# Kernel optimization log

Measured on AMD Instinct MI355X. Metric: run time of the kernel, lower is better.

Reference implementation:

```python
import jax, jax.numpy as jnp
import numpy as np

HIDDEN = 2048
NUM_HEADS = 16
HEAD_DIM = HIDDEN // NUM_HEADS


def setup_inputs() -> dict:
    key = jax.random.key(0)
    k1, k2, k3 = jax.random.split(key, 3)
    hidden_states = jax.random.normal(k1, (4, 2048, HIDDEN), dtype=jnp.float32)
    # torch Linear weight is (out, in); y = x @ W.T. Store transposed (in, out).
    w_qkv = jax.random.normal(k2, (HIDDEN, 3 * HIDDEN), dtype=jnp.float32) * (HIDDEN ** -0.5)
    w_o = jax.random.normal(k3, (HIDDEN, HIDDEN), dtype=jnp.float32) * (HIDDEN ** -0.5)
    return {"hidden_states": hidden_states, "w_qkv": w_qkv, "w_o": w_o}


def reference(hidden_states, w_qkv, w_o):
    B, S, _ = hidden_states.shape
    qkv = hidden_states @ w_qkv  # (B, S, 3*HIDDEN)
    # Faithful to torch .view: row-major reshape straight to (B, H, S, 3*head_dim)
    qkv = qkv.reshape(B, NUM_HEADS, S, 3 * HEAD_DIM)
    q, k, v = jnp.split(qkv, 3, axis=-1)  # each (B, H, S, head_dim)
    scores = jnp.einsum('bhsd,bhtd->bhst', q, k) / (HEAD_DIM ** 0.5)
    probs = jax.nn.softmax(scores, axis=-1)
    attn = jnp.einsum('bhst,bhtd->bhsd', probs, v)  # (B, H, S, head_dim)
    # Faithful to torch .reshape(B, S, hidden) without transpose
    attn = attn.reshape(B, S, HIDDEN)
    return attn @ w_o
```

## Files before the change

kernel.cpp:

```cpp
#include <hip/hip_runtime.h>
#include <stdint.h>

#define DEVINL __device__ __forceinline__

typedef __attribute__((ext_vector_type(8))) __bf16 bf16x8;
typedef __attribute__((ext_vector_type(4))) float f32x4;
typedef __attribute__((ext_vector_type(16))) float f32x16;

static constexpr int HID  = 2048;
static constexpr int NQ   = 6144;
static constexpr int SEQ  = 2048;
static constexpr int NB   = 4;
static constexpr int MTOT = NB * SEQ;

DEVINL unsigned short f2bf(float f) {
  union { float f; uint32_t u; } x; x.f = f;
  uint32_t r = x.u + 0x7fffu + ((x.u >> 16) & 1u);
  return (unsigned short)(r >> 16);
}

typedef const __attribute__((address_space(1))) void gvoid_t;
typedef __attribute__((address_space(3))) void svoid_t;

DEVINL void gload_lds16(const void* g, void* s) {
  __builtin_amdgcn_global_load_lds((gvoid_t*)(uintptr_t)g,
                                   (svoid_t*)(uint32_t)(uintptr_t)s,
                                   16, 0, 0);
}


__global__ void k_cvt(const float* __restrict__ in, unsigned short* __restrict__ out, int n4) {
  int i = blockIdx.x * blockDim.x + threadIdx.x;
  if (i >= n4) return;
  float4 v = ((const float4*)in)[i];
  ushort4 o;
  o.x = f2bf(v.x); o.y = f2bf(v.y); o.z = f2bf(v.z); o.w = f2bf(v.w);
  ((ushort4*)out)[i] = o;
}

__global__ void k_transpose_cvt(const float* __restrict__ in, unsigned short* __restrict__ out,
                                int R, int C) {
  __shared__ float tile[32][33];
  int c0 = blockIdx.x * 32, r0 = blockIdx.y * 32;
  int tx = threadIdx.x & 31, ty = threadIdx.x >> 5;
  #pragma unroll
  for (int i = 0; i < 32; i += 8)
    tile[ty + i][tx] = in[(size_t)(r0 + ty + i) * C + (c0 + tx)];
  __syncthreads();
  #pragma unroll
  for (int i = 0; i < 32; i += 8)
    out[(size_t)(c0 + ty + i) * R + (r0 + tx)] = f2bf(tile[tx][ty + i]);
}


template <int OUT_BF16>
__global__ __launch_bounds__(256, 2) void k_gemm(const unsigned short* __restrict__ A,
                                                 const unsigned short* __restrict__ BT,
                                                 void* __restrict__ Cout,
                                                 int M, int N, int K) {
  __shared__ unsigned short As[128 * 64];
  __shared__ unsigned short Bs[128 * 64];
  const int tid = threadIdx.x;
  const int w = tid >> 6, l = tid & 63;
  const int lane16 = l & 15, lgrp = l >> 4;
  const int bn = blockIdx.x, bm = blockIdx.y;
  const int wr = w >> 1, wc = w & 1;
  const int srow = l >> 3;
  const int sk = (l & 7) * 8;

  f32x4 acc[4][4] = {};

  for (int k0 = 0; k0 < K; k0 += 64) {
    #pragma unroll
    for (int i = 0; i < 4; ++i) {
      const int chunk = i * 4 + w;
      const int row = chunk * 8 + srow;
      gload_lds16(A  + (size_t)(bm * 128 + row) * K + k0 + sk, As + chunk * 512);
      gload_lds16(BT + (size_t)(bn * 128 + row) * K + k0 + sk, Bs + chunk * 512);
    }
    __syncthreads();
    #pragma unroll
    for (int kk = 0; kk < 2; ++kk) {
      bf16x8 af[4], bfr[4];
      #pragma unroll
      for (int m = 0; m < 4; ++m)
        af[m] = *(const bf16x8*)(As + (wr * 64 + m * 16 + lane16) * 64 + kk * 32 + lgrp * 8);
      #pragma unroll
      for (int n = 0; n < 4; ++n)
        bfr[n] = *(const bf16x8*)(Bs + (wc * 64 + n * 16 + lane16) * 64 + kk * 32 + lgrp * 8);
      #pragma unroll
      for (int m = 0; m < 4; ++m)
        #pragma unroll
        for (int n = 0; n < 4; ++n)
          acc[m][n] = __builtin_amdgcn_mfma_f32_16x16x32_bf16(af[m], bfr[n], acc[m][n], 0, 0, 0);
    }
    __syncthreads();
  }

  const int row0 = bm * 128 + wr * 64;
  const int col0 = bn * 128 + wc * 64;
  #pragma unroll
  for (int m = 0; m < 4; ++m) {
    #pragma unroll
    for (int n = 0; n < 4; ++n) {
      const int col = col0 + n * 16 + lane16;
      #pragma unroll
      for (int r = 0; r < 4; ++r) {
        const int row = row0 + m * 16 + lgrp * 4 + r;
        if (OUT_BF16)
          ((unsigned short*)Cout)[(size_t)row * N + col] = f2bf(acc[m][n][r]);
        else
          ((float*)Cout)[(size_t)row * N + col] = acc[m][n][r];
      }
    }
  }
}

__global__ void k_build_vt(const unsigned short* __restrict__ QKV, unsigned short* __restrict__ Vt) {
  const int head = blockIdx.y;
  const int s_rel = blockIdx.x;
  const int b = head >> 4, h = head & 15;
  const int d = threadIdx.x;
  const unsigned short* src = QKV + (size_t)(b * SEQ + h * 128 + s_rel) * NQ + 256 + d;
  unsigned short vals[16];
  #pragma unroll
  for (int c1 = 0; c1 < 16; ++c1) vals[c1] = src[c1 * 384];
  unsigned short* dst = Vt + ((size_t)head * 128 + d) * SEQ + s_rel * 16;
  #pragma unroll
  for (int c1 = 0; c1 < 16; ++c1) dst[c1] = vals[c1];
}

__global__ __launch_bounds__(256, 2) void k_attn(const unsigned short* __restrict__ QKV,
                                                 const unsigned short* __restrict__ Vt,
                                                 unsigned short* __restrict__ ATT) {
  __shared__ unsigned short Ks[2][64 * 128];
  __shared__ unsigned short Vs[2][128 * 64];
  const int tid = threadIdx.x, w = tid >> 6, l = tid & 63;
  const int l32 = l & 31, hi = l >> 5;
  const int qt = blockIdx.x, head = blockIdx.y;
  const int b = head >> 4, h = head & 15;
  const float scale = 0.08838834764831845f;
  const float THR = 8.0f / 0.08838834764831845f;
  const int base_row = b * SEQ + h * 128;

  const int s = qt * 128 + w * 32 + l32;
  bf16x8 qf[8];
  {
    const unsigned short* qrow = QKV + (size_t)(base_row + (s >> 4)) * NQ + (s & 15) * 384;
    #pragma unroll
    for (int dsl = 0; dsl < 8; ++dsl)
      qf[dsl] = *(const bf16x8*)(qrow + dsl * 16 + hi * 8);
  }

  f32x16 oacc[4] = {};
  float mrun = -1e30f, lrun = 0.0f;

  #define STAGE_KV(bb, kv0)                                                              \
    {                                                                                    \
      _Pragma("unroll")                                                                  \
      for (int i = 0; i < 4; ++i) {                                                      \
        const int chunk = i * 4 + w;                                                     \
        const int r = chunk * 4 + (l >> 4);                                              \
        const int colsw = ((l & 15) ^ (r & 15)) * 8;                                     \
        gload_lds16(QKV + (size_t)(base_row + ((kv0) >> 4) + (r >> 4)) * NQ              \
                        + (r & 15) * 384 + 128 + colsw,                                  \
                    &Ks[bb][chunk * 512]);                                               \
      }                                                                                  \
      _Pragma("unroll")                                                                  \
      for (int i = 0; i < 4; ++i) {                                                      \
        const int chunk = i * 4 + w;                                                     \
        const int dr = chunk * 8 + (l >> 3);                                             \
        const int colsw = ((l & 7) ^ (dr & 7)) * 8;                                      \
        gload_lds16(Vt + ((size_t)head * 128 + dr) * SEQ + (kv0) + colsw,                \
                    &Vs[bb][chunk * 512]);                                               \
      }                                                                                  \
    }

  STAGE_KV(0, 0);
  __syncthreads();

  int buf = 0;
  for (int kv0 = 0; kv0 < SEQ; kv0 += 64) {
    if (kv0 + 64 < SEQ) STAGE_KV(buf ^ 1, kv0 + 64);

    f32x16 sacc[2] = {};
    __builtin_amdgcn_s_setprio(1);
    #pragma unroll
    for (int kvf = 0; kvf < 2; ++kvf) {
      const int row = kvf * 32 + l32;
      const unsigned short* kbase = &Ks[buf][row * 128];
      const int rs = (row & 15) << 3;
      #pragma unroll
      for (int dsl = 0; dsl < 8; ++dsl) {
        bf16x8 kf = *(const bf16x8*)(kbase + ((dsl * 16 + hi * 8) ^ rs));
        sacc[kvf] = __builtin_amdgcn_mfma_f32_32x32x16_bf16(kf, qf[dsl], sacc[kvf], 0, 0, 0);
      }
    }
    __builtin_amdgcn_s_setprio(0);

    float mx[16];
    #pragma unroll
    for (int r = 0; r < 16; ++r) mx[r] = fmaxf(sacc[0][r], sacc[1][r]);
    #pragma unroll
    for (int st = 8; st >= 1; st >>= 1)
      #pragma unroll
      for (int r = 0; r < st; ++r) mx[r] = fmaxf(mx[r], mx[r + st]);
    float pmax = fmaxf(mx[0], __shfl_xor(mx[0], 32));

    if (!__all(pmax - mrun <= THR)) {
      const float mnew = fmaxf(mrun, pmax);
      const float corr = __expf((mrun - mnew) * scale);
      #pragma unroll
      for (int df = 0; df < 4; ++df)
        #pragma unroll
        for (int r = 0; r < 16; ++r) oacc[df][r] *= corr;
      lrun *= corr;
      mrun = mnew;
    }

    float ps[16];
    #pragma unroll
    for (int r = 0; r < 16; ++r) {
      const float p0 = __expf((sacc[0][r] - mrun) * scale);
      const float p1 = __expf((sacc[1][r] - mrun) * scale);
      sacc[0][r] = p0; sacc[1][r] = p1;
      ps[r] = p0 + p1;
    }
    #pragma unroll
    for (int st = 8; st >= 1; st >>= 1)
      #pragma unroll
      for (int r = 0; r < st; ++r) ps[r] += ps[r + st];
    lrun += ps[0] + __shfl_xor(ps[0], 32);

    bf16x8 pf[4];
    #pragma unroll
    for (int f = 0; f < 2; ++f) {
      unsigned int c0, c1, c2, c3, c4, c5, c6, c7;
      asm("v_cvt_pk_bf16_f32 %0, %1, %2" : "=v"(c0) : "v"(sacc[f][0]),  "v"(sacc[f][1]));
      asm("v_cvt_pk_bf16_f32 %0, %1, %2" : "=v"(c1) : "v"(sacc[f][2]),  "v"(sacc[f][3]));
      asm("v_cvt_pk_bf16_f32 %0, %1, %2" : "=v"(c2) : "v"(sacc[f][4]),  "v"(sacc[f][5]));
      asm("v_cvt_pk_bf16_f32 %0, %1, %2" : "=v"(c3) : "v"(sacc[f][6]),  "v"(sacc[f][7]));
      asm("v_cvt_pk_bf16_f32 %0, %1, %2" : "=v"(c4) : "v"(sacc[f][8]),  "v"(sacc[f][9]));
      asm("v_cvt_pk_bf16_f32 %0, %1, %2" : "=v"(c5) : "v"(sacc[f][10]), "v"(sacc[f][11]));
      asm("v_cvt_pk_bf16_f32 %0, %1, %2" : "=v"(c6) : "v"(sacc[f][12]), "v"(sacc[f][13]));
      asm("v_cvt_pk_bf16_f32 %0, %1, %2" : "=v"(c7) : "v"(sacc[f][14]), "v"(sacc[f][15]));
      asm("v_permlane32_swap_b32 %0, %1" : "+v"(c0), "+v"(c2));
      asm("v_permlane32_swap_b32 %0, %1" : "+v"(c1), "+v"(c3));
      asm("v_permlane32_swap_b32 %0, %1" : "+v"(c4), "+v"(c6));
      asm("v_permlane32_swap_b32 %0, %1" : "+v"(c5), "+v"(c7));
      union { unsigned int u[4]; bf16x8 v; } u0, u1;
      u0.u[0] = c0; u0.u[1] = c1; u0.u[2] = c2; u0.u[3] = c3;
      u1.u[0] = c4; u1.u[1] = c5; u1.u[2] = c6; u1.u[3] = c7;
      pf[2 * f] = u0.v; pf[2 * f + 1] = u1.v;
    }

    __builtin_amdgcn_s_setprio(1);
    #pragma unroll
    for (int ks = 0; ks < 4; ++ks) {
      #pragma unroll
      for (int df = 0; df < 4; ++df) {
        const int row = df * 32 + l32;
        bf16x8 vf = *(const bf16x8*)(&Vs[buf][row * 64 + (((ks * 16 + hi * 8) ^ ((row & 7) << 3)))]);
        oacc[df] = __builtin_amdgcn_mfma_f32_32x32x16_bf16(vf, pf[ks], oacc[df], 0, 0, 0);
      }
    }
    __builtin_amdgcn_s_setprio(0);

    __syncthreads();
    buf ^= 1;
  }

  const float inv = 1.0f / lrun;
  unsigned short* orow = ATT + (size_t)(base_row + (s >> 4)) * HID + (s & 15) * 128;
  #pragma unroll
  for (int df = 0; df < 4; ++df) {
    #pragma unroll
    for (int k = 0; k < 4; ++k) {
      ushort4 o;
      o.x = f2bf(oacc[df][4 * k + 0] * inv);
      o.y = f2bf(oacc[df][4 * k + 1] * inv);
      o.z = f2bf(oacc[df][4 * k + 2] * inv);
      o.w = f2bf(oacc[df][4 * k + 3] * inv);
      *(ushort4*)(orow + df * 32 + 8 * k + 4 * hi) = o;
    }
  }
}


extern "C" void kernel_launch(void* const* d_in, const int* in_sizes, int n_in,
                              void* d_out, int out_size, void* d_ws, size_t ws_size,
                              hipStream_t stream) {
  const float* X    = (const float*)d_in[0];
  const float* Wqkv = (const float*)d_in[1];
  const float* Wo   = (const float*)d_in[2];
  float* OUT = (float*)d_out;

  char* ws = (char*)d_ws;
  constexpr size_t SZ_QKV   = (size_t)MTOT * NQ * 2;
  constexpr size_t SZ_XBF   = (size_t)MTOT * HID * 2;
  constexpr size_t SZ_WQKVT = (size_t)NQ * HID * 2;
  constexpr size_t SZ_WOT   = (size_t)HID * HID * 2;
  constexpr size_t SZ_VT    = (size_t)64 * 128 * SEQ * 2;
  unsigned short* QKV   = (unsigned short*)(ws);
  unsigned short* Xbf   = (unsigned short*)(ws + SZ_QKV);
  unsigned short* WqkvT = (unsigned short*)(ws + SZ_QKV + SZ_XBF);
  unsigned short* WoT   = (unsigned short*)(ws + SZ_QKV + SZ_XBF + SZ_WQKVT);
  unsigned short* Vt    = (unsigned short*)(ws + SZ_QKV + SZ_XBF + SZ_WQKVT + SZ_WOT);
  unsigned short* ATT   = (unsigned short*)(ws + SZ_QKV + SZ_XBF + SZ_WQKVT + SZ_WOT + SZ_VT);

  k_cvt<<<(MTOT * HID / 4 + 255) / 256, 256, 0, stream>>>(X, Xbf, MTOT * HID / 4);
  k_transpose_cvt<<<dim3(NQ / 32, HID / 32), 256, 0, stream>>>(Wqkv, WqkvT, HID, NQ);
  k_transpose_cvt<<<dim3(HID / 32, HID / 32), 256, 0, stream>>>(Wo, WoT, HID, HID);
  k_gemm<1><<<dim3(NQ / 128, MTOT / 128), 256, 0, stream>>>(Xbf, WqkvT, QKV, MTOT, NQ, HID);
  k_build_vt<<<dim3(128, 64), 128, 0, stream>>>(QKV, Vt);
  k_attn<<<dim3(16, 64), 256, 0, stream>>>(QKV, Vt, ATT);
  k_gemm<0><<<dim3(HID / 128, MTOT / 128), 256, 0, stream>>>(ATT, WoT, OUT, MTOT, HID, HID);
}
```

Baseline: 550.6 us.

## Replace GEMM with 256x256 double-buffered swizzled LDS pipeline kernel

Both projection GEMMs move from a simple 128x128 single-buffered kernel to a 256x256 tile kernel with 8 waves. The new kernel double-buffers LDS in quarter regions and issues global-to-LDS loads for later K tiles while MFMAs run on the current ones. It also XOR-swizzles LDS slots to avoid bank conflicts, remaps workgroup IDs for better L2 locality, and raises wave priority around the MFMA blocks. The aim is to hide memory latency and raise operand reuse. The cost is much more LDS (128KB per block), more registers for a 128-entry accumulator, and complex barrier ordering that could limit occupancy.

```diff
diff --git a/kernel.cpp b/kernel.cpp
--- a/kernel.cpp
+++ b/kernel.cpp
@@ -53,64 +53,167 @@
 }
 
 
+DEVINL void stage_half(const unsigned short* __restrict__ G, size_t row_base, int K, int k0,
+                       unsigned short* region, int tid, int isA, int lohi) {
+  #pragma unroll
+  for (int j = 0; j < 2; ++j) {
+    const int lin = j * 512 + tid;
+    const int rr = lin >> 3;
+    const int slot = (lin & 7) ^ (rr & 7);
+    int grow;
+    if (isA) grow = (lohi ? 64 : 0) + (rr & 63) + ((rr >> 6) << 7);
+    else     grow = ((rr >> 5) << 6) + (lohi ? 32 : 0) + (rr & 31);
+    gload_lds16(G + (row_base + (size_t)grow) * K + k0 + slot * 8,
+                region + (size_t)(j * 512 + ((tid >> 6) << 6)) * 8);
+  }
+}
+
+DEVINL bf16x8 lds_frag(const unsigned short* region, int rr, int ks, int lgrp) {
+  return *(const bf16x8*)(region + rr * 64 + (((ks * 4 + lgrp) ^ (rr & 7)) * 8));
+}
+
 template <int OUT_BF16>
-__global__ __launch_bounds__(256, 2) void k_gemm(const unsigned short* __restrict__ A,
-                                                 const unsigned short* __restrict__ BT,
-                                                 void* __restrict__ Cout,
-                                                 int M, int N, int K) {
-  __shared__ unsigned short As[128 * 64];
-  __shared__ unsigned short Bs[128 * 64];
+__global__ __launch_bounds__(512, 2) void k_gemm256(const unsigned short* __restrict__ A,
+                                                    const unsigned short* __restrict__ BT,
+                                                    void* __restrict__ Cout,
+                                                    int M, int N, int K) {
+  __shared__ unsigned short lds[2][4][128 * 64];
   const int tid = threadIdx.x;
   const int w = tid >> 6, l = tid & 63;
   const int lane16 = l & 15, lgrp = l >> 4;
-  const int bn = blockIdx.x, bm = blockIdx.y;
-  const int wr = w >> 1, wc = w & 1;
-  const int srow = l >> 3;
-  const int sk = (l & 7) * 8;
-
-  f32x4 acc[4][4] = {};
-
-  for (int k0 = 0; k0 < K; k0 += 64) {
-    #pragma unroll
-    for (int i = 0; i < 4; ++i) {
-      const int chunk = i * 4 + w;
-      const int row = chunk * 8 + srow;
-      gload_lds16(A  + (size_t)(bm * 128 + row) * K + k0 + sk, As + chunk * 512);
-      gload_lds16(BT + (size_t)(bn * 128 + row) * K + k0 + sk, Bs + chunk * 512);
-    }
-    __syncthreads();
-    #pragma unroll
-    for (int kk = 0; kk < 2; ++kk) {
-      bf16x8 af[4], bfr[4];
-      #pragma unroll
-      for (int m = 0; m < 4; ++m)
-        af[m] = *(const bf16x8*)(As + (wr * 64 + m * 16 + lane16) * 64 + kk * 32 + lgrp * 8);
-      #pragma unroll
-      for (int n = 0; n < 4; ++n)
-        bfr[n] = *(const bf16x8*)(Bs + (wc * 64 + n * 16 + lane16) * 64 + kk * 32 + lgrp * 8);
-      #pragma unroll
-      for (int m = 0; m < 4; ++m)
-        #pragma unroll
-        for (int n = 0; n < 4; ++n)
-          acc[m][n] = __builtin_amdgcn_mfma_f32_16x16x32_bf16(af[m], bfr[n], acc[m][n], 0, 0, 0);
-    }
-    __syncthreads();
-  }
-
-  const int row0 = bm * 128 + wr * 64;
-  const int col0 = bn * 128 + wc * 64;
-  #pragma unroll
-  for (int m = 0; m < 4; ++m) {
-    #pragma unroll
-    for (int n = 0; n < 4; ++n) {
-      const int col = col0 + n * 16 + lane16;
+  const int wm = w >> 2, wn = w & 3;
+
+  const int nbn = N >> 8;
+  const int nwg = gridDim.x;
+  int wgid = blockIdx.x;
+  wgid = (wgid & 7) * (nwg >> 3) + (wgid >> 3);
+  const int bm = wgid / nbn, bn = wgid % nbn;
+
+  const size_t arb = (size_t)bm * 256, brb = (size_t)bn * 256;
+  const int NT = K >> 6;
+
+  stage_half(A,  arb, K, 0,  &lds[0][0][0], tid, 1, 0);
+  stage_half(BT, brb, K, 0,  &lds[0][2][0], tid, 0, 0);
+  stage_half(BT, brb, K, 0,  &lds[0][3][0], tid, 0, 1);
+  stage_half(A,  arb, K, 0,  &lds[0][1][0], tid, 1, 1);
+  stage_half(A,  arb, K, 64, &lds[1][0][0], tid, 1, 0);
+  stage_half(BT, brb, K, 64, &lds[1][2][0], tid, 0, 0);
+  stage_half(BT, brb, K, 64, &lds[1][3][0], tid, 0, 1);
+  asm volatile("s_waitcnt vmcnt(6)" ::: "memory");
+  __builtin_amdgcn_s_barrier();
+
+  f32x4 acc[8][4] = {};
+  bf16x8 af[4][2], blo[2][2], bhi[2][2];
+
+  for (int i = 0; i < NT / 2; ++i) {
+    const int t1 = 2 * i + 1;
+    const int t2k = ((2 * i + 2 < NT) ? 2 * i + 2 : NT - 2) * 64;
+    const int t3k = ((2 * i + 3 < NT) ? 2 * i + 3 : NT - 1) * 64;
+
+    #pragma unroll
+    for (int half = 0; half < 2; ++half) {
+      const unsigned short* Ralo = &lds[half][0][0];
+      const unsigned short* Rahi = &lds[half][1][0];
+      const unsigned short* Rblo = &lds[half][2][0];
+      const unsigned short* Rbhi = &lds[half][3][0];
+
+      #pragma unroll
+      for (int mf = 0; mf < 4; ++mf) {
+        const int rr = wm * 64 + mf * 16 + lane16;
+        #pragma unroll
+        for (int ks = 0; ks < 2; ++ks) af[mf][ks] = lds_frag(Ralo, rr, ks, lgrp);
+      }
+      #pragma unroll
+      for (int nf = 0; nf < 2; ++nf) {
+        const int rr = wn * 32 + nf * 16 + lane16;
+        #pragma unroll
+        for (int ks = 0; ks < 2; ++ks) blo[nf][ks] = lds_frag(Rblo, rr, ks, lgrp);
+      }
+      if (half == 0) stage_half(A, arb, K, t1 * 64, &lds[1][1][0], tid, 1, 1);
+      else           stage_half(A, arb, K, t2k,     &lds[0][1][0], tid, 1, 1);
+      __builtin_amdgcn_s_barrier();
+      __builtin_amdgcn_s_setprio(1);
+      #pragma unroll
+      for (int ks = 0; ks < 2; ++ks)
+        #pragma unroll
+        for (int mf = 0; mf < 4; ++mf)
+          #pragma unroll
+          for (int nf = 0; nf < 2; ++nf)
+            acc[mf][nf] = __builtin_amdgcn_mfma_f32_16x16x32_bf16(af[mf][ks], blo[nf][ks], acc[mf][nf], 0, 0, 0);
+      __builtin_amdgcn_s_setprio(0);
+      __builtin_amdgcn_s_barrier();
+
+      #pragma unroll
+      for (int nf = 0; nf < 2; ++nf) {
+        const int rr = wn * 32 + nf * 16 + lane16;
+        #pragma unroll
+        for (int ks = 0; ks < 2; ++ks) bhi[nf][ks] = lds_frag(Rbhi, rr, ks, lgrp);
+      }
+      if (half == 0) stage_half(A, arb, K, t2k, &lds[0][0][0], tid, 1, 0);
+      else           stage_half(A, arb, K, t3k, &lds[1][0][0], tid, 1, 0);
+      __builtin_amdgcn_s_barrier();
+      __builtin_amdgcn_s_setprio(1);
+      #pragma unroll
+      for (int ks = 0; ks < 2; ++ks)
+        #pragma unroll
+        for (int mf = 0; mf < 4; ++mf)
+          #pragma unroll
+          for (int nf = 0; nf < 2; ++nf)
+            acc[mf][nf + 2] = __builtin_amdgcn_mfma_f32_16x16x32_bf16(af[mf][ks], bhi[nf][ks], acc[mf][nf + 2], 0, 0, 0);
+      __builtin_amdgcn_s_setprio(0);
+      __builtin_amdgcn_s_barrier();
+
+      #pragma unroll
+      for (int mf = 0; mf < 4; ++mf) {
+        const int rr = wm * 64 + mf * 16 + lane16;
+        #pragma unroll
+        for (int ks = 0; ks < 2; ++ks) af[mf][ks] = lds_frag(Rahi, rr, ks, lgrp);
+      }
+      if (half == 0) stage_half(BT, brb, K, t2k, &lds[0][2][0], tid, 0, 0);
+      else           stage_half(BT, brb, K, t3k, &lds[1][2][0], tid, 0, 0);
+      __builtin_amdgcn_s_barrier();
+      __builtin_amdgcn_s_setprio(1);
+      #pragma unroll
+      for (int ks = 0; ks < 2; ++ks)
+        #pragma unroll
+        for (int mf = 0; mf < 4; ++mf)
+          #pragma unroll
+          for (int nf = 0; nf < 2; ++nf)
+            acc[mf + 4][nf] = __builtin_amdgcn_mfma_f32_16x16x32_bf16(af[mf][ks], blo[nf][ks], acc[mf + 4][nf], 0, 0, 0);
+      __builtin_amdgcn_s_setprio(0);
+      __builtin_amdgcn_s_barrier();
+
+      if (half == 0) stage_half(BT, brb, K, t2k, &lds[0][3][0], tid, 0, 1);
+      else           stage_half(BT, brb, K, t3k, &lds[1][3][0], tid, 0, 1);
+      __builtin_amdgcn_s_barrier();
+      __builtin_amdgcn_s_setprio(1);
+      #pragma unroll
+      for (int ks = 0; ks < 2; ++ks)
+        #pragma unroll
+        for (int mf = 0; mf < 4; ++mf)
+          #pragma unroll
+          for (int nf = 0; nf < 2; ++nf)
+            acc[mf + 4][nf + 2] = __builtin_amdgcn_mfma_f32_16x16x32_bf16(af[mf][ks], bhi[nf][ks], acc[mf + 4][nf + 2], 0, 0, 0);
+      __builtin_amdgcn_s_setprio(0);
+      asm volatile("s_waitcnt vmcnt(6)" ::: "memory");
+      __builtin_amdgcn_s_barrier();
+    }
+  }
+
+  const size_t row0 = (size_t)bm * 256 + wm * 128;
+  const int col0 = bn * 256 + wn * 64;
+  #pragma unroll
+  for (int mf = 0; mf < 8; ++mf) {
+    #pragma unroll
+    for (int nf = 0; nf < 4; ++nf) {
+      const int col = col0 + nf * 16 + lane16;
       #pragma unroll
       for (int r = 0; r < 4; ++r) {
-        const int row = row0 + m * 16 + lgrp * 4 + r;
+        const size_t row = row0 + mf * 16 + lgrp * 4 + r;
         if (OUT_BF16)
-          ((unsigned short*)Cout)[(size_t)row * N + col] = f2bf(acc[m][n][r]);
+          ((unsigned short*)Cout)[row * N + col] = f2bf(acc[mf][nf][r]);
         else
-          ((float*)Cout)[(size_t)row * N + col] = acc[m][n][r];
+          ((float*)Cout)[row * N + col] = acc[mf][nf][r];
       }
     }
   }
@@ -311,8 +414,8 @@
   k_cvt<<<(MTOT * HID / 4 + 255) / 256, 256, 0, stream>>>(X, Xbf, MTOT * HID / 4);
   k_transpose_cvt<<<dim3(NQ / 32, HID / 32), 256, 0, stream>>>(Wqkv, WqkvT, HID, NQ);
   k_transpose_cvt<<<dim3(HID / 32, HID / 32), 256, 0, stream>>>(Wo, WoT, HID, HID);
-  k_gemm<1><<<dim3(NQ / 128, MTOT / 128), 256, 0, stream>>>(Xbf, WqkvT, QKV, MTOT, NQ, HID);
+  k_gemm256<1><<<(MTOT / 256) * (NQ / 256), 512, 0, stream>>>(Xbf, WqkvT, QKV, MTOT, NQ, HID);
   k_build_vt<<<dim3(128, 64), 128, 0, stream>>>(QKV, Vt);
   k_attn<<<dim3(16, 64), 256, 0, stream>>>(QKV, Vt, ATT);
-  k_gemm<0><<<dim3(HID / 128, MTOT / 128), 256, 0, stream>>>(ATT, WoT, OUT, MTOT, HID, HID);
-}
+  k_gemm256<0><<<(MTOT / 256) * (HID / 256), 512, 0, stream>>>(ATT, WoT, OUT, MTOT, HID, HID);
+}
```

Result: slower. 818.3 us (+48.6%).

## Enlarge GEMM tile to 256x128 and XOR-swizzle LDS layout

Applied to the files above, without the earlier changes.

Replaces the 128x128 GEMM with a 256x128 tile in which each wave owns 64 rows across all 128 columns, doubling per-wave accumulators to 4x8 MFMA fragments. This raises arithmetic intensity per LDS load and halves the number of blocks. Global-to-LDS loads and fragment reads now use an XOR swizzle on the 16-byte column slot to avoid LDS bank conflicts. The trade-off is higher register pressure (128 accumulator floats per lane) and fewer blocks for the output projection GEMM, which may hurt occupancy.

```diff
diff --git a/kernel.cpp b/kernel.cpp
--- a/kernel.cpp
+++ b/kernel.cpp
@@ -54,63 +54,72 @@
 
 
 template <int OUT_BF16>
-__global__ __launch_bounds__(256, 2) void k_gemm(const unsigned short* __restrict__ A,
-                                                 const unsigned short* __restrict__ BT,
-                                                 void* __restrict__ Cout,
-                                                 int M, int N, int K) {
-  __shared__ unsigned short As[128 * 64];
+__global__ __launch_bounds__(256, 2) void k_gemm2(const unsigned short* __restrict__ A,
+                                                  const unsigned short* __restrict__ BT,
+                                                  void* __restrict__ Cout,
+                                                  int M, int N, int K) {
+  __shared__ unsigned short As[256 * 64];
   __shared__ unsigned short Bs[128 * 64];
   const int tid = threadIdx.x;
   const int w = tid >> 6, l = tid & 63;
   const int lane16 = l & 15, lgrp = l >> 4;
   const int bn = blockIdx.x, bm = blockIdx.y;
-  const int wr = w >> 1, wc = w & 1;
   const int srow = l >> 3;
-  const int sk = (l & 7) * 8;
-
-  f32x4 acc[4][4] = {};
+  const int gslot = (l & 7) ^ (l >> 3);
+
+  f32x4 acc[4][8] = {};
 
   for (int k0 = 0; k0 < K; k0 += 64) {
+    #pragma unroll
+    for (int i = 0; i < 8; ++i) {
+      const int chunk = i * 4 + w;
+      const int row = chunk * 8 + srow;
+      gload_lds16(A + (size_t)(bm * 256 + row) * K + k0 + gslot * 8, As + chunk * 512);
+    }
     #pragma unroll
     for (int i = 0; i < 4; ++i) {
       const int chunk = i * 4 + w;
       const int row = chunk * 8 + srow;
-      gload_lds16(A  + (size_t)(bm * 128 + row) * K + k0 + sk, As + chunk * 512);
-      gload_lds16(BT + (size_t)(bn * 128 + row) * K + k0 + sk, Bs + chunk * 512);
+      gload_lds16(BT + (size_t)(bn * 128 + row) * K + k0 + gslot * 8, Bs + chunk * 512);
     }
     __syncthreads();
+
     #pragma unroll
     for (int kk = 0; kk < 2; ++kk) {
-      bf16x8 af[4], bfr[4];
-      #pragma unroll
-      for (int m = 0; m < 4; ++m)
-        af[m] = *(const bf16x8*)(As + (wr * 64 + m * 16 + lane16) * 64 + kk * 32 + lgrp * 8);
-      #pragma unroll
-      for (int n = 0; n < 4; ++n)
-        bfr[n] = *(const bf16x8*)(Bs + (wc * 64 + n * 16 + lane16) * 64 + kk * 32 + lgrp * 8);
-      #pragma unroll
-      for (int m = 0; m < 4; ++m)
+      bf16x8 af[4], bfr[8];
+      #pragma unroll
+      for (int mf = 0; mf < 4; ++mf) {
+        const int row = w * 64 + mf * 16 + lane16;
+        af[mf] = *(const bf16x8*)(As + row * 64 + (((kk * 4 + lgrp) ^ (row & 7)) * 8));
+      }
+      #pragma unroll
+      for (int nf = 0; nf < 8; ++nf) {
+        const int row = nf * 16 + lane16;
+        bfr[nf] = *(const bf16x8*)(Bs + row * 64 + (((kk * 4 + lgrp) ^ (row & 7)) * 8));
+      }
+      #pragma unroll
+      for (int mf = 0; mf < 4; ++mf)
         #pragma unroll
-        for (int n = 0; n < 4; ++n)
-          acc[m][n] = __builtin_amdgcn_mfma_f32_16x16x32_bf16(af[m], bfr[n], acc[m][n], 0, 0, 0);
+        for (int nf = 0; nf < 8; ++nf)
+          acc[mf][nf] = __builtin_amdgcn_mfma_f32_16x16x32_bf16(af[mf], bfr[nf], acc[mf][nf], 0, 0, 0);
     }
     __syncthreads();
   }
 
-  const int row0 = bm * 128 + wr * 64;
-  const int col0 = bn * 128 + wc * 64;
-  #pragma unroll
-  for (int m = 0; m < 4; ++m) {
-    #pragma unroll
-    for (int n = 0; n < 4; ++n) {
-      const int col = col0 + n * 16 + lane16;
+  const size_t row0 = (size_t)bm * 256 + w * 64;
+  const int col0 = bn * 128;
+  #pragma unroll
+  for (int mf = 0; mf < 4; ++mf) {
+    #pragma unroll
+    for (int nf = 0; nf < 8; ++nf) {
+      const int col = col0 + nf * 16 + lane16;
       #pragma unroll
       for (int r = 0; r < 4; ++r) {
-        const int row = row0 + m * 16 + lgrp * 4 + r;
+        const size_t row = row0 + mf * 16 + lgrp * 4 + r;
         if (OUT_BF16)
-          ((unsigned short*)Cout)[(size_t)row * N + col] = f2bf(acc[m][n][r]);
+          ((unsigned short*)Cout)[row * N + col] = f2bf(acc[mf][nf][r]);
         else
-          ((float*)Cout)[(size_t)row * N + col] = acc[m][n][r];
+          ((float*)Cout)[row * N + col] = acc[mf][nf][r];
       }
     }
   }
@@ -311,8 +320,8 @@
   k_cvt<<<(MTOT * HID / 4 + 255) / 256, 256, 0, stream>>>(X, Xbf, MTOT * HID / 4);
   k_transpose_cvt<<<dim3(NQ / 32, HID / 32), 256, 0, stream>>>(Wqkv, WqkvT, HID, NQ);
   k_transpose_cvt<<<dim3(HID / 32, HID / 32), 256, 0, stream>>>(Wo, WoT, HID, HID);
-  k_gemm<1><<<dim3(NQ / 128, MTOT / 128), 256, 0, stream>>>(Xbf, WqkvT, QKV, MTOT, NQ, HID);
+  k_gemm2<1><<<dim3(NQ / 128, MTOT / 256), 256, 0, stream>>>(Xbf, WqkvT, QKV, MTOT, NQ, HID);
   k_build_vt<<<dim3(128, 64), 128, 0, stream>>>(QKV, Vt);
   k_attn<<<dim3(16, 64), 256, 0, stream>>>(QKV, Vt, ATT);
-  k_gemm<0><<<dim3(HID / 128, MTOT / 128), 256, 0, stream>>>(ATT, WoT, OUT, MTOT, HID, HID);
-}
+  k_gemm2<0><<<dim3(HID / 128, MTOT / 256), 256, 0, stream>>>(ATT, WoT, OUT, MTOT, HID, HID);
+}
```

Result: faster. 477.1 us (-13.4%).
